# Performance work log

Measured on AMD Instinct MI355X. Metric: run time of the kernel, lower is better.

## Reference

```python
import jax, jax.numpy as jnp
import numpy as np


def _mlp(x, W0, b0, W1, b1, W2, b2, W3, b3):
    # nlayers=4 MLP: 3->128->128->128->3 with ReLU between layers
    h = jax.nn.relu(x @ W0 + b0)
    h = jax.nn.relu(h @ W1 + b1)
    h = jax.nn.relu(h @ W2 + b2)
    return h @ W3 + b3


def setup_inputs() -> dict:
    key = jax.random.key(0)
    ks = jax.random.split(key, 8)
    B, Nc, Nt, Dx, Dy, H = 8, 1024, 1024, 3, 32, 128
    s = lambda fan: 1.0 / np.sqrt(fan)
    return {
        "xc": jax.random.normal(ks[0], (B, Nc, Dx), jnp.float32),
        "yc": jax.random.normal(ks[1], (B, Nc, Dy), jnp.float32),
        "xt": jax.random.normal(ks[2], (B, Nt, Dx), jnp.float32),
        "W0": jax.random.normal(ks[3], (Dx, H), jnp.float32) * s(Dx),
        "b0": jnp.zeros((H,), jnp.float32),
        "W1": jax.random.normal(ks[4], (H, H), jnp.float32) * s(H),
        "b1": jnp.zeros((H,), jnp.float32),
        "W2": jax.random.normal(ks[5], (H, H), jnp.float32) * s(H),
        "b2": jnp.zeros((H,), jnp.float32),
        "W3": jax.random.normal(ks[6], (H, Dx), jnp.float32) * s(H),
        "b3": jnp.zeros((Dx,), jnp.float32),
    }


def reference(xc, yc, xt, W0, b0, W1, b1, W2, b2, W3, b3):
    # sigmas: per-target, per-coordinate positive scales  (B, Nt, Dx)
    sig = jnp.exp(_mlp(xt, W0, b0, W1, b1, W2, b2, W3, b3))
    # squared differences (B, Nc, Nt, Dx), scaled and reduced over Dx
    A = (xc[:, :, None, :] - xt[:, None, :, :]) ** 2
    P = -(A * sig[:, None, :, :]).sum(axis=3)        # (B, Nc, Nt)
    S = jax.nn.softmax(P, axis=1)                    # softmax over context
    # weighted average of context values: (B, Nt, Dy)
    return jnp.einsum("bnd,bnt->btd", yc, S)
```

## Files before the change

kernel.cpp:

```cpp
#include <hip/hip_runtime.h>
#include <math.h>

#define BB 8
#define NCC 1024
#define NTT 1024
#define HH 128
#define DYY 32
#define NTB 16
#define LOG2E 1.44269504088896340736f

typedef _Float16 half8 __attribute__((ext_vector_type(8)));
typedef float f32x4 __attribute__((ext_vector_type(4)));

#define HB 0
#define RED 2112
#define SIGL 8192
#define SMEM_SZ 8240
#define CMB 0
#define SL 4224
#define HSTRIDE 132

__global__ __launch_bounds__(512, 2) void k_fused(const float* __restrict__ xc,
                                                  const float* __restrict__ yc,
                                                  const float* __restrict__ xt,
                                                  const float* __restrict__ W0,
                                                  const float* __restrict__ b0,
                                                  const float* __restrict__ W1,
                                                  const float* __restrict__ b1,
                                                  const float* __restrict__ W2,
                                                  const float* __restrict__ b2,
                                                  const float* __restrict__ W3,
                                                  const float* __restrict__ b3,
                                                  float* __restrict__ out) {
    const int tid = threadIdx.x;
    const int phys = blockIdx.x;
    const int bid = (phys & 7) * 64 + (phys >> 3);
    const int t0 = bid * NTB;
    const int b = bid >> 6;
    const int wv = tid >> 6;
    const int lane = tid & 63;

    __shared__ float smem[SMEM_SZ];

    const float4* __restrict__ xcG4 = (const float4*)(xc + (size_t)b * NCC * 3);

    const int jg = tid >> 4;
    const int p = tid & 15;
    const int j0 = jg * 4;
    float* hrow = smem + HB + p * HSTRIDE;

    {
        const float* xr = xt + (size_t)(t0 + p) * 3;
        const float x0 = xr[0], x1 = xr[1], x2 = xr[2];
        const float4* W0v = (const float4*)W0;
        const float4 w0a = W0v[jg], w0b = W0v[32 + jg], w0c = W0v[64 + jg];
        const float4 bb0 = ((const float4*)b0)[jg];
        float4 h0;
        h0.x = fmaxf(fmaf(x0, w0a.x, fmaf(x1, w0b.x, fmaf(x2, w0c.x, bb0.x))), 0.f);
        h0.y = fmaxf(fmaf(x0, w0a.y, fmaf(x1, w0b.y, fmaf(x2, w0c.y, bb0.y))), 0.f);
        h0.z = fmaxf(fmaf(x0, w0a.z, fmaf(x1, w0b.z, fmaf(x2, w0c.z, bb0.z))), 0.f);
        h0.w = fmaxf(fmaf(x0, w0a.w, fmaf(x1, w0b.w, fmaf(x2, w0c.w, bb0.w))), 0.f);
        *(float4*)(hrow + j0) = h0;
    }
    __syncthreads();

    {
        const int mtl = lane & 15;
        const int mg = lane >> 4;
        const int jcol = wv * 16 + mtl;

#pragma unroll
        for (int l = 0; l < 2; ++l) {
            const float* __restrict__ Wg = (l == 0) ? W1 : W2;
            const float* __restrict__ bi = (l == 0) ? b1 : b2;
            f32x4 dac;
            {
                const float bj = bi[jcol];
                dac[0] = bj; dac[1] = bj; dac[2] = bj; dac[3] = bj;
            }
            float w[8];
#pragma unroll
            for (int i = 0; i < 8; ++i) w[i] = Wg[(mg * 8 + i) * HH + jcol];
#pragma unroll
            for (int c = 0; c < 4; ++c) {
                float wn[8];
                if (c < 3) {
#pragma unroll
                    for (int i = 0; i < 8; ++i)
                        wn[i] = Wg[((c + 1) * 32 + mg * 8 + i) * HH + jcol];
                }
                float hv[8];
                *(float4*)hv =
                    *(const float4*)(smem + HB + mtl * HSTRIDE + c * 32 + mg * 8);
                *(float4*)(hv + 4) =
                    *(const float4*)(smem + HB + mtl * HSTRIDE + c * 32 + mg * 8 + 4);
                half8 a0, a1, bf0, bf1;
#pragma unroll
                for (int i = 0; i < 8; ++i) {
                    const _Float16 ah = (_Float16)hv[i];
                    a0[i] = ah;
                    a1[i] = (_Float16)(hv[i] - (float)ah);
                    const _Float16 wh = (_Float16)w[i];
                    bf0[i] = wh;
                    bf1[i] = (_Float16)(w[i] - (float)wh);
                }
                dac = __builtin_amdgcn_mfma_f32_16x16x32_f16(a0, bf0, dac, 0, 0, 0);
                dac = __builtin_amdgcn_mfma_f32_16x16x32_f16(a0, bf1, dac, 0, 0, 0);
                dac = __builtin_amdgcn_mfma_f32_16x16x32_f16(a1, bf0, dac, 0, 0, 0);
                if (c < 3) {
#pragma unroll
                    for (int i = 0; i < 8; ++i) w[i] = wn[i];
                }
            }
            __syncthreads();
#pragma unroll
            for (int r = 0; r < 4; ++r)
                smem[HB + (mg * 4 + r) * HSTRIDE + jcol] = fmaxf(dac[r], 0.f);
            __syncthreads();
        }
    }

    {
        const float4 o4 = *(const float4*)(hrow + j0);
        const float4* W3v = (const float4*)W3;
        const float4 wr0 = W3v[jg * 3 + 0];
        const float4 wr1 = W3v[jg * 3 + 1];
        const float4 wr2 = W3v[jg * 3 + 2];
        float p0 = o4.x * wr0.x + o4.y * wr0.w + o4.z * wr1.z + o4.w * wr2.y;
        float p1 = o4.x * wr0.y + o4.y * wr1.x + o4.z * wr1.w + o4.w * wr2.z;
        float p2 = o4.x * wr0.z + o4.y * wr1.y + o4.z * wr2.x + o4.w * wr2.w;
        p0 += __shfl_xor(p0, 16, 64);
        p0 += __shfl_xor(p0, 32, 64);
        p1 += __shfl_xor(p1, 16, 64);
        p1 += __shfl_xor(p1, 32, 64);
        p2 += __shfl_xor(p2, 16, 64);
        p2 += __shfl_xor(p2, 32, 64);
        if (lane < 16) {
            smem[RED + wv * 48 + lane * 3 + 0] = p0;
            smem[RED + wv * 48 + lane * 3 + 1] = p1;
            smem[RED + wv * 48 + lane * 3 + 2] = p2;
        }
    }
    __syncthreads();
    if (tid < 48) {
        const int r = tid / 3, cix = tid - r * 3;
        float v = b3[cix];
#pragma unroll
        for (int g2 = 0; g2 < 8; ++g2) v += smem[RED + g2 * 48 + r * 3 + cix];
        smem[SIGL + r * 3 + cix] = __expf(v) * LOG2E;
    }
    __syncthreads();

    const int tl = lane & 15;
    const int g = lane >> 4;
    const int sd = lane & 31;
    const int snr = lane >> 5;

    const float s0 = smem[SIGL + tl * 3 + 0];
    const float s1 = smem[SIGL + tl * 3 + 1];
    const float s2 = smem[SIGL + tl * 3 + 2];
    const float* ar = xt + (size_t)(t0 + tl) * 3;
    const float a0 = ar[0], a1 = ar[1], a2 = ar[2];

    float* warena = smem + wv * 1024;
    _Float16* ycT = (_Float16*)warena;
    float* xcw = warena + 640;

    if (lane < 48) {
        float4 tx0 = xcG4[wv * 96 + lane];
        float4 tx1 = xcG4[wv * 96 + 48 + lane];
        ((float4*)xcw)[lane] = tx0;
        ((float4*)xcw)[lane + 48] = tx1;
    }

    const float* ycol = yc + (size_t)b * NCC * DYY + (size_t)(wv * 128) * DYY + sd;
    float ld[16];
#define YLOAD(C)                                                               \
    _Pragma("unroll") for (int q = 0; q < 16; ++q)                             \
        ld[q] = ycol[(size_t)((C) * 32 + (q >> 3) * 16 + snr * 8 + (q & 7)) * DYY];
#define YWRITE()                                                               \
    do {                                                                       \
        _Pragma("unroll") for (int r = 0; r < 2; ++r) {                        \
            half8 pk;                                                          \
            _Pragma("unroll") for (int j = 0; j < 8; ++j)                      \
                pk[j] = (_Float16)ld[r * 8 + j];                               \
            *(half8*)(ycT + sd * 40 + r * 16 + snr * 8) = pk;                  \
        }                                                                      \
    } while (0)

    YLOAD(0);
    YWRITE();

    f32x4 acc0 = {0.f, 0.f, 0.f, 0.f};
    f32x4 acc1 = {0.f, 0.f, 0.f, 0.f};
    float l = 0.f;

#pragma unroll
    for (int c = 0; c < 4; ++c) {
        if (c < 3) YLOAD(c + 1);

        float xv[24];
        {
            const float4* xr4 = (const float4*)(xcw + (c * 32 + g * 8) * 3);
#pragma unroll
            for (int q = 0; q < 6; ++q) *(float4*)(xv + q * 4) = xr4[q];
        }
        half8 af;
#pragma unroll
        for (int i = 0; i < 8; ++i) {
            const float d0 = xv[i * 3 + 0] - a0;
            const float d1 = xv[i * 3 + 1] - a1;
            const float d2 = xv[i * 3 + 2] - a2;
            const float pp = fmaf(s0, d0 * d0, fmaf(s1, d1 * d1, s2 * (d2 * d2)));
            const _Float16 eh = (_Float16)exp2f(-pp);
            af[i] = eh;
            l += (float)eh;
        }
        const half8 bf0 = *(const half8*)(ycT + tl * 40 + g * 8);
        const half8 bf1 = *(const half8*)(ycT + (16 + tl) * 40 + g * 8);
        acc0 = __builtin_amdgcn_mfma_f32_16x16x32_f16(af, bf0, acc0, 0, 0, 0);
        acc1 = __builtin_amdgcn_mfma_f32_16x16x32_f16(af, bf1, acc1, 0, 0, 0);

        if (c < 3) YWRITE();
    }

    l += __shfl_xor(l, 16, 64);
    l += __shfl_xor(l, 32, 64);

    __syncthreads();
#pragma unroll
    for (int r = 0; r < 4; ++r) {
        smem[CMB + wv * 528 + (g * 4 + r) * 33 + tl] = acc0[r];
        smem[CMB + wv * 528 + (g * 4 + r) * 33 + 16 + tl] = acc1[r];
    }
    if (lane < 16) smem[SL + wv * 16 + lane] = l;
    __syncthreads();
    {
        const int t = tid >> 5, d = tid & 31;
        float s = 0.f, ls = 0.f;
#pragma unroll
        for (int w = 0; w < 8; ++w) {
            s += smem[CMB + w * 528 + t * 33 + d];
            ls += smem[SL + w * 16 + t];
        }
        out[(size_t)(t0 + t) * DYY + d] = s / ls;
    }
#undef YLOAD
#undef YWRITE
}

extern "C" void kernel_launch(void* const* d_in, const int* in_sizes, int n_in,
                              void* d_out, int out_size, void* d_ws, size_t ws_size,
                              hipStream_t stream) {
    const float* xc = (const float*)d_in[0];
    const float* yc = (const float*)d_in[1];
    const float* xt = (const float*)d_in[2];
    const float* W0 = (const float*)d_in[3];
    const float* b0 = (const float*)d_in[4];
    const float* W1 = (const float*)d_in[5];
    const float* b1 = (const float*)d_in[6];
    const float* W2 = (const float*)d_in[7];
    const float* b2 = (const float*)d_in[8];
    const float* W3 = (const float*)d_in[9];
    const float* b3 = (const float*)d_in[10];
    float* out = (float*)d_out;

    k_fused<<<dim3(BB * NTT / NTB), dim3(512), 0, stream>>>(xc, yc, xt, W0, b0,
                                                            W1, b1, W2, b2, W3,
                                                            b3, out);
}
```

Measured before the change: 85.54 us.

## Load yc fragments directly into MFMA B registers, drop LDS transpose staging

Removes the per-wave LDS staging and transpose of yc. Each lane now gathers its own MFMA B-operand elements straight from global memory and converts them to fp16 in registers. The xc tile load moves into the MLP prologue region before the first barrier, and shared memory shrinks. This cuts LDS traffic and the software pipeline, but the global reads become strided and less coalesced, and their latency is no longer overlapped by prefetch.

```diff
diff --git a/kernel.cpp b/kernel.cpp
--- a/kernel.cpp
+++ b/kernel.cpp
@@ -14,8 +14,9 @@
 
 #define HB 0
 #define RED 2112
-#define SIGL 8192
-#define SMEM_SZ 8240
+#define XCW 2496
+#define SIGL 5568
+#define SMEM_SZ 5616
 #define CMB 0
 #define SL 4224
 #define HSTRIDE 132
@@ -62,6 +63,16 @@
         h0.w = fmaxf(fmaf(x0, w0a.w, fmaf(x1, w0b.w, fmaf(x2, w0c.w, bb0.w))), 0.f);
         *(float4*)(hrow + j0) = h0;
     }
+
+    {
+        float* xcw = smem + XCW + wv * 384;
+        if (lane < 48) {
+            float4 tx0 = xcG4[wv * 96 + lane];
+            float4 tx1 = xcG4[wv * 96 + 48 + lane];
+            ((float4*)xcw)[lane] = tx0;
+            ((float4*)xcw)[lane + 48] = tx1;
+        }
+    }
     __syncthreads();
 
     {
@@ -153,8 +164,6 @@
 
     const int tl = lane & 15;
     const int g = lane >> 4;
-    const int sd = lane & 31;
-    const int snr = lane >> 5;
 
     const float s0 = smem[SIGL + tl * 3 + 0];
     const float s1 = smem[SIGL + tl * 3 + 1];
@@ -162,34 +171,9 @@
     const float* ar = xt + (size_t)(t0 + tl) * 3;
     const float a0 = ar[0], a1 = ar[1], a2 = ar[2];
 
-    float* warena = smem + wv * 1024;
-    _Float16* ycT = (_Float16*)warena;
-    float* xcw = warena + 640;
-
-    if (lane < 48) {
-        float4 tx0 = xcG4[wv * 96 + lane];
-        float4 tx1 = xcG4[wv * 96 + 48 + lane];
-        ((float4*)xcw)[lane] = tx0;
-        ((float4*)xcw)[lane + 48] = tx1;
-    }
-
-    const float* ycol = yc + (size_t)b * NCC * DYY + (size_t)(wv * 128) * DYY + sd;
-    float ld[16];
-#define YLOAD(C)                                                               \
-    _Pragma("unroll") for (int q = 0; q < 16; ++q)                             \
-        ld[q] = ycol[(size_t)((C) * 32 + (q >> 3) * 16 + snr * 8 + (q & 7)) * DYY];
-#define YWRITE()                                                               \
-    do {                                                                       \
-        _Pragma("unroll") for (int r = 0; r < 2; ++r) {                        \
-            half8 pk;                                                          \
-            _Pragma("unroll") for (int j = 0; j < 8; ++j)                      \
-                pk[j] = (_Float16)ld[r * 8 + j];                               \
-            *(half8*)(ycT + sd * 40 + r * 16 + snr * 8) = pk;                  \
-        }                                                                      \
-    } while (0)
-
-    YLOAD(0);
-    YWRITE();
+    const float* xcw = smem + XCW + wv * 384;
+    const float* __restrict__ yB =
+        yc + (size_t)b * NCC * DYY + (size_t)(wv * 128 + g * 8) * DYY + tl;
 
     f32x4 acc0 = {0.f, 0.f, 0.f, 0.f};
     f32x4 acc1 = {0.f, 0.f, 0.f, 0.f};
@@ -197,7 +181,12 @@
 
 #pragma unroll
     for (int c = 0; c < 4; ++c) {
-        if (c < 3) YLOAD(c + 1);
+        float by0[8], by1[8];
+#pragma unroll
+        for (int i = 0; i < 8; ++i) {
+            by0[i] = yB[(c * 32 + i) * DYY];
+            by1[i] = yB[(c * 32 + i) * DYY + 16];
+        }
 
         float xv[24];
         {
@@ -205,7 +194,7 @@
 #pragma unroll
             for (int q = 0; q < 6; ++q) *(float4*)(xv + q * 4) = xr4[q];
         }
-        half8 af;
+        half8 af, bf0, bf1;
 #pragma unroll
         for (int i = 0; i < 8; ++i) {
             const float d0 = xv[i * 3 + 0] - a0;
@@ -215,13 +204,11 @@
             const _Float16 eh = (_Float16)exp2f(-pp);
             af[i] = eh;
             l += (float)eh;
-        }
-        const half8 bf0 = *(const half8*)(ycT + tl * 40 + g * 8);
-        const half8 bf1 = *(const half8*)(ycT + (16 + tl) * 40 + g * 8);
+            bf0[i] = (_Float16)by0[i];
+            bf1[i] = (_Float16)by1[i];
+        }
         acc0 = __builtin_amdgcn_mfma_f32_16x16x32_f16(af, bf0, acc0, 0, 0, 0);
         acc1 = __builtin_amdgcn_mfma_f32_16x16x32_f16(af, bf1, acc1, 0, 0, 0);
-
-        if (c < 3) YWRITE();
     }
 
     l += __shfl_xor(l, 16, 64);
@@ -245,8 +232,6 @@
         }
         out[(size_t)(t0 + t) * DYY + d] = s / ls;
     }
-#undef YLOAD
-#undef YWRITE
 }
 
 extern "C" void kernel_launch(void* const* d_in, const int* in_sizes, int n_in,
```

Result: no change. 85.67 us (+0.2%).
